# Performance work log

Measured on AMD Instinct MI355X. Metric: run time of the kernel, lower is better.

The kernel has to match this reference:

```python
import jax, jax.numpy as jnp
import numpy as np

H, W, C = 56, 56, 192
WS, SS = 7, 3          # window_size, shift_size
NH, HD = 6, 32         # num_heads, head_dim
N = WS * WS            # tokens per window = 49
HIDDEN = 4 * C
EPS = 1e-5


def _rel_pos_index():
    coords = np.stack(np.meshgrid(np.arange(WS), np.arange(WS), indexing='ij'))  # (2,ws,ws)
    flat = coords.reshape(2, -1)
    rel = flat[:, :, None] - flat[:, None, :]            # (2,N,N)
    rel = rel.transpose(1, 2, 0)
    rel[:, :, 0] += WS - 1
    rel[:, :, 1] += WS - 1
    rel[:, :, 0] *= 2 * WS - 1
    return rel.sum(-1)                                   # (N,N) int


def _attn_mask():
    img = np.zeros((H, W))
    cnt = 0
    for hs in (slice(0, -WS), slice(-WS, -SS), slice(-SS, None)):
        for ws_ in (slice(0, -WS), slice(-WS, -SS), slice(-SS, None)):
            img[hs, ws_] = cnt
            cnt += 1
    mw = img.reshape(H // WS, WS, W // WS, WS).transpose(0, 2, 1, 3).reshape(-1, N)  # (nW,N)
    diff = mw[:, None, :] - mw[:, :, None]
    return np.where(diff != 0, -100.0, 0.0).astype(np.float32)  # (nW,N,N)


REL_IDX = jnp.asarray(_rel_pos_index())
ATTN_MASK = jnp.asarray(_attn_mask())


def _ln(x, w, b):
    mu = x.mean(-1, keepdims=True)
    var = ((x - mu) ** 2).mean(-1, keepdims=True)
    return (x - mu) * jax.lax.rsqrt(var + EPS) * w + b


def _window_partition(x):
    # (B,H,W,C) -> (B*nW, N, C)
    B = x.shape[0]
    x = x.reshape(B, H // WS, WS, W // WS, WS, C)
    x = x.transpose(0, 1, 3, 2, 4, 5)
    return x.reshape(-1, N, C)


def _window_reverse(win, B):
    # (B*nW, N, C) -> (B,H,W,C)
    x = win.reshape(B, H // WS, W // WS, WS, WS, C)
    x = x.transpose(0, 1, 3, 2, 4, 5)
    return x.reshape(B, H, W, C)


def setup_inputs() -> dict:
    key = jax.random.key(0)
    ks = jax.random.split(key, 16)
    s = 0.02
    return {
        'x': jax.random.normal(ks[0], (64, H * W, C), jnp.float32),
        'norm1_w': jnp.ones((C,), jnp.float32),
        'norm1_b': jnp.zeros((C,), jnp.float32),
        'qkv_w': jax.random.normal(ks[1], (C, 3 * C), jnp.float32) * s,
        'qkv_b': jnp.zeros((3 * C,), jnp.float32),
        'rpb': jax.random.normal(ks[2], ((2 * WS - 1) ** 2, NH), jnp.float32) * s,
        'proj_w': jax.random.normal(ks[3], (C, C), jnp.float32) * s,
        'proj_b': jnp.zeros((C,), jnp.float32),
        'norm2_w': jnp.ones((C,), jnp.float32),
        'norm2_b': jnp.zeros((C,), jnp.float32),
        'fc1_w': jax.random.normal(ks[4], (C, HIDDEN), jnp.float32) * s,
        'fc1_b': jnp.zeros((HIDDEN,), jnp.float32),
        'fc2_w': jax.random.normal(ks[5], (HIDDEN, C), jnp.float32) * s,
        'fc2_b': jnp.zeros((C,), jnp.float32),
    }


def reference(x, norm1_w, norm1_b, qkv_w, qkv_b, rpb, proj_w, proj_b,
              norm2_w, norm2_b, fc1_w, fc1_b, fc2_w, fc2_b):
    B = x.shape[0]
    nW = (H // WS) * (W // WS)
    shortcut = x
    h = _ln(x, norm1_w, norm1_b).reshape(B, H, W, C)
    # cyclic shift
    h = jnp.roll(h, shift=(-SS, -SS), axis=(1, 2))
    xw = _window_partition(h)                                   # (B*nW, N, C)
    # windowed MHA
    qkv = (xw @ qkv_w + qkv_b).reshape(-1, N, 3, NH, HD).transpose(2, 0, 3, 1, 4)
    q, k, v = qkv[0], qkv[1], qkv[2]                            # (Bn, NH, N, HD)
    scale = HD ** -0.5
    attn = jnp.einsum('bhnd,bhmd->bhnm', q * scale, k)          # (Bn, NH, N, N)
    bias = rpb[REL_IDX.reshape(-1)].reshape(N, N, NH).transpose(2, 0, 1)
    attn = attn + bias[None]
    attn = attn.reshape(B, nW, NH, N, N) + ATTN_MASK[None, :, None]
    attn = jax.nn.softmax(attn.reshape(-1, NH, N, N), axis=-1)
    out = jnp.einsum('bhnm,bhmd->bhnd', attn, v)
    out = out.transpose(0, 2, 1, 3).reshape(-1, N, C)
    out = out @ proj_w + proj_b
    # reverse windows + un-shift
    h = _window_reverse(out, B)
    h = jnp.roll(h, shift=(SS, SS), axis=(1, 2)).reshape(B, H * W, C)
    x = shortcut + h
    # MLP (exact GELU, as torch nn.GELU default)
    m = _ln(x, norm2_w, norm2_b)
    m = jax.nn.gelu(m @ fc1_w + fc1_b, approximate=False)
    m = m @ fc2_w + fc2_b
    return x + m
```

## Files before the change

### kernel.cpp

```cpp
#include <hip/hip_runtime.h>
#include <hip/hip_bf16.h>

typedef __hip_bfloat16 bf16;
typedef __attribute__((ext_vector_type(8))) short short8;
typedef __attribute__((ext_vector_type(4))) float floatx4;

__device__ __forceinline__ floatx4 mfma16(short8 a, short8 b, floatx4 c) {
  return __builtin_amdgcn_mfma_f32_16x16x32_bf16(a, b, c, 0, 0, 0);
}

__device__ __forceinline__ float wave_sum(float v) {
#pragma unroll
  for (int off = 1; off < 64; off <<= 1) v += __shfl_xor(v, off);
  return v;
}

__global__ __launch_bounds__(256) void k_wt(const float* __restrict__ w,
                                            bf16* __restrict__ wt, int K, int N) {
  int id = blockIdx.x * 256 + threadIdx.x;
  if (id < K * N) {
    int n = id / K;
    int k = id - n * K;
    wt[id] = __float2bfloat16(w[(long)k * N + n]);
  }
}

template <bool GATHER>
__global__ __launch_bounds__(256) void k_ln(const float* __restrict__ xin,
                                            const float* __restrict__ w,
                                            const float* __restrict__ b,
                                            bf16* __restrict__ out) {
  const int lane = threadIdx.x & 63;
  const long row = (long)blockIdx.x * 4 + (threadIdx.x >> 6);
  long srow;
  if (GATHER) {
    int win = (int)(row / 49);
    int token = (int)(row - (long)win * 49);
    int bimg = win >> 6, wi = (win & 63) >> 3, wj = win & 7;
    int ti = token / 7, tj = token - ti * 7;
    int h = wi * 7 + ti + 3; if (h >= 56) h -= 56;
    int ww = wj * 7 + tj + 3; if (ww >= 56) ww -= 56;
    srow = (long)bimg * 3136 + h * 56 + ww;
  } else {
    srow = row;
  }
  const float* src = xin + srow * 192;
  float v0 = src[lane], v1 = src[lane + 64], v2 = src[lane + 128];
  float mu = wave_sum(v0 + v1 + v2) * (1.f / 192.f);
  float d0 = v0 - mu, d1 = v1 - mu, d2 = v2 - mu;
  float var = wave_sum(d0 * d0 + d1 * d1 + d2 * d2) * (1.f / 192.f);
  float rs = rsqrtf(var + 1e-5f);
  bf16* dst = out + row * 192;
  dst[lane]       = __float2bfloat16(d0 * rs * w[lane] + b[lane]);
  dst[lane + 64]  = __float2bfloat16(d1 * rs * w[lane + 64] + b[lane + 64]);
  dst[lane + 128] = __float2bfloat16(d2 * rs * w[lane + 128] + b[lane + 128]);
}

template <int EPI>
__global__ __launch_bounds__(256) void k_gemm(const bf16* __restrict__ A,
                                              const bf16* __restrict__ Bt,
                                              const float* __restrict__ bias,
                                              bf16* __restrict__ Cbf,
                                              float* __restrict__ Cfp,
                                              const float* __restrict__ res,
                                              int Ncols, int K, long row0) {
  __shared__ __align__(16) bf16 As[64 * 40];
  __shared__ __align__(16) bf16 Bs[64 * 40];
  const int t = threadIdx.x;
  const int lane = t & 63, wid = t >> 6;
  const int lanelo = lane & 15, quad = lane >> 4;
  const long m0 = (long)blockIdx.x * 64;
  const int n0 = blockIdx.y * 64;
  const int wm = (wid >> 1) * 32, wn = (wid & 1) * 32;
  const int srow = t >> 2, sch = (t & 3) * 8;

  floatx4 acc[2][2];
#pragma unroll
  for (int i = 0; i < 2; i++)
#pragma unroll
    for (int j = 0; j < 2; j++) acc[i][j] = (floatx4){0.f, 0.f, 0.f, 0.f};

  const bf16* Ap = A + (m0 + srow) * K + sch;
  const bf16* Bp = Bt + (long)(n0 + srow) * K + sch;

  for (int k0 = 0; k0 < K; k0 += 32) {
    __syncthreads();
    *(uint4*)(&As[srow * 40 + sch]) = *(const uint4*)(Ap + k0);
    *(uint4*)(&Bs[srow * 40 + sch]) = *(const uint4*)(Bp + k0);
    __syncthreads();
    short8 a0 = *(const short8*)(&As[(wm + lanelo) * 40 + quad * 8]);
    short8 a1 = *(const short8*)(&As[(wm + 16 + lanelo) * 40 + quad * 8]);
    short8 b0 = *(const short8*)(&Bs[(wn + lanelo) * 40 + quad * 8]);
    short8 b1 = *(const short8*)(&Bs[(wn + 16 + lanelo) * 40 + quad * 8]);
    acc[0][0] = mfma16(a0, b0, acc[0][0]);
    acc[0][1] = mfma16(a0, b1, acc[0][1]);
    acc[1][0] = mfma16(a1, b0, acc[1][0]);
    acc[1][1] = mfma16(a1, b1, acc[1][1]);
  }

#pragma unroll
  for (int mi = 0; mi < 2; mi++) {
#pragma unroll
    for (int reg = 0; reg < 4; reg++) {
      const long r = m0 + wm + mi * 16 + quad * 4 + reg;
      long orow = r;
      if (EPI == 2) {
        const long rg = row0 + r;
        int win = (int)(rg / 49);
        int token = (int)(rg - (long)win * 49);
        int bimg = win >> 6, wi = (win & 63) >> 3, wj = win & 7;
        int ti = token / 7, tj = token - ti * 7;
        int h = wi * 7 + ti + 3; if (h >= 56) h -= 56;
        int ww = wj * 7 + tj + 3; if (ww >= 56) ww -= 56;
        orow = (long)bimg * 3136 + h * 56 + ww;
      }
#pragma unroll
      for (int ni = 0; ni < 2; ni++) {
        const int c = n0 + wn + ni * 16 + lanelo;
        float v = acc[mi][ni][reg] + bias[c];
        if (EPI == 0) {
          Cbf[r * Ncols + c] = __float2bfloat16(v);
        } else if (EPI == 1) {
          v = 0.5f * v * (1.f + erff(v * 0.70710678118654752f));
          Cbf[r * Ncols + c] = __float2bfloat16(v);
        } else if (EPI == 2) {
          Cfp[orow * 192 + c] = v + res[orow * 192 + c];
        } else {
          Cfp[r * 192 + c] = v + res[r * 192 + c];
        }
      }
    }
  }
}

__global__ __launch_bounds__(256, 2) void k_attn(const bf16* __restrict__ qkv,
                                                 const float* __restrict__ rpb,
                                                 bf16* __restrict__ out) {
  __shared__ __align__(16) bf16 smem[4 * 7424];
  const int t = threadIdx.x, lane = t & 63, wid = t >> 6;
  const int lanelo = lane & 15, quad = lane >> 4;
  const int unit = blockIdx.x * 4 + wid;
  const int win = unit / 6, head = unit - win * 6;
  bf16* Qs = smem + wid * 7424;
  bf16* Ks = Qs + 2560;
  bf16* Vt = Qs + 5120;
  bf16* Ps = Qs;
  const long rowbase = (long)win * 49;
  const bf16* base = qkv + rowbase * 576 + head * 32;

  for (int idx = lane; idx < 196; idx += 64) {
    int tok = idx >> 2, ch = (idx & 3) * 8;
    *(uint4*)(&Qs[tok * 40 + ch]) = *(const uint4*)(base + (long)tok * 576 + ch);
    *(uint4*)(&Ks[tok * 40 + ch]) = *(const uint4*)(base + (long)tok * 576 + 192 + ch);
    union { uint4 u; bf16 h[8]; } tv;
    tv.u = *(const uint4*)(base + (long)tok * 576 + 384 + ch);
#pragma unroll
    for (int jj = 0; jj < 8; jj++) Vt[(ch + jj) * 72 + tok] = tv.h[jj];
  }
  for (int idx = lane; idx < 480; idx += 64) {
    int d = idx / 15, c = 49 + (idx - d * 15);
    Vt[d * 72 + c] = __float2bfloat16(0.f);
  }
  __syncthreads();

  floatx4 aS[4][4];
#pragma unroll
  for (int mi = 0; mi < 4; mi++)
#pragma unroll
    for (int ni = 0; ni < 4; ni++) aS[mi][ni] = (floatx4){0.f, 0.f, 0.f, 0.f};
  {
    short8 aq[4], bk[4];
#pragma unroll
    for (int mi = 0; mi < 4; mi++)
      aq[mi] = *(const short8*)(&Qs[(mi * 16 + lanelo) * 40 + quad * 8]);
#pragma unroll
    for (int ni = 0; ni < 4; ni++)
      bk[ni] = *(const short8*)(&Ks[(ni * 16 + lanelo) * 40 + quad * 8]);
#pragma unroll
    for (int mi = 0; mi < 4; mi++)
#pragma unroll
      for (int ni = 0; ni < 4; ni++) aS[mi][ni] = mfma16(aq[mi], bk[ni], aS[mi][ni]);
  }

  const int w_in = win & 63, wiw = w_in >> 3, wjw = w_in & 7;
  int cTi[4], cTj[4], cLab[4];
  bool cval[4];
#pragma unroll
  for (int ni = 0; ni < 4; ni++) {
    int j = ni * 16 + lanelo;
    cval[ni] = (j < 49);
    if (j > 48) j = 48;
    int ti = j / 7, tj = j - ti * 7;
    int rr = wiw * 7 + ti, cc = wjw * 7 + tj;
    cTi[ni] = ti;
    cTj[ni] = tj;
    cLab[ni] = ((rr < 49) ? 0 : (rr < 53 ? 1 : 2)) * 3 +
               ((cc < 49) ? 0 : (cc < 53 ? 1 : 2));
  }

  const float scale = 0.17677669529663687f;
  float rinv[16];
#pragma unroll
  for (int mi = 0; mi < 4; mi++) {
#pragma unroll
    for (int reg = 0; reg < 4; reg++) {
      int i = mi * 16 + quad * 4 + reg;
      if (i > 48) i = 48;
      int ti = i / 7, tj = i - ti * 7;
      int rr = wiw * 7 + ti, cc = wjw * 7 + tj;
      int rlab = ((rr < 49) ? 0 : (rr < 53 ? 1 : 2)) * 3 +
                 ((cc < 49) ? 0 : (cc < 53 ? 1 : 2));
      float sv[4];
      float mx = -1e30f;
#pragma unroll
      for (int ni = 0; ni < 4; ni++) {
        float s;
        if (cval[ni]) {
          int ridx = (ti - cTi[ni] + 6) * 13 + (tj - cTj[ni] + 6);
          float bb = rpb[ridx * 6 + head];
          if (rlab != cLab[ni]) bb -= 100.f;
          s = aS[mi][ni][reg] * scale + bb;
        } else {
          s = -1e30f;
        }
        sv[ni] = s;
        mx = fmaxf(mx, s);
      }
      mx = fmaxf(mx, __shfl_xor(mx, 1));
      mx = fmaxf(mx, __shfl_xor(mx, 2));
      mx = fmaxf(mx, __shfl_xor(mx, 4));
      mx = fmaxf(mx, __shfl_xor(mx, 8));
      float sum = 0.f;
#pragma unroll
      for (int ni = 0; ni < 4; ni++) {
        float p = __expf(sv[ni] - mx);
        sv[ni] = p;
        sum += p;
      }
      sum += __shfl_xor(sum, 1);
      sum += __shfl_xor(sum, 2);
      sum += __shfl_xor(sum, 4);
      sum += __shfl_xor(sum, 8);
      rinv[mi * 4 + reg] = 1.f / sum;
#pragma unroll
      for (int ni = 0; ni < 4; ni++) aS[mi][ni][reg] = sv[ni];
    }
  }
  __syncthreads();

#pragma unroll
  for (int mi = 0; mi < 4; mi++)
#pragma unroll
    for (int ni = 0; ni < 4; ni++)
#pragma unroll
      for (int reg = 0; reg < 4; reg++) {
        int i = mi * 16 + quad * 4 + reg, j = ni * 16 + lanelo;
        Ps[i * 72 + j] = __float2bfloat16(aS[mi][ni][reg]);
      }
  __syncthreads();

  floatx4 aO[4][2];
#pragma unroll
  for (int mi = 0; mi < 4; mi++)
#pragma unroll
    for (int ni = 0; ni < 2; ni++) aO[mi][ni] = (floatx4){0.f, 0.f, 0.f, 0.f};
#pragma unroll
  for (int k0 = 0; k0 < 64; k0 += 32) {
    short8 ap[4], bv[2];
#pragma unroll
    for (int mi = 0; mi < 4; mi++)
      ap[mi] = *(const short8*)(&Ps[(mi * 16 + lanelo) * 72 + k0 + quad * 8]);
#pragma unroll
    for (int ni = 0; ni < 2; ni++)
      bv[ni] = *(const short8*)(&Vt[(ni * 16 + lanelo) * 72 + k0 + quad * 8]);
#pragma unroll
    for (int mi = 0; mi < 4; mi++)
#pragma unroll
      for (int ni = 0; ni < 2; ni++) aO[mi][ni] = mfma16(ap[mi], bv[ni], aO[mi][ni]);
  }

#pragma unroll
  for (int mi = 0; mi < 4; mi++)
#pragma unroll
    for (int reg = 0; reg < 4; reg++) {
      int i = mi * 16 + quad * 4 + reg;
      if (i < 49) {
        float rv = rinv[mi * 4 + reg];
#pragma unroll
        for (int ni = 0; ni < 2; ni++) {
          int d = ni * 16 + lanelo;
          out[(rowbase + i) * 192 + head * 32 + d] =
              __float2bfloat16(aO[mi][ni][reg] * rv);
        }
      }
    }
}

extern "C" void kernel_launch(void* const* d_in, const int* in_sizes, int n_in,
                              void* d_out, int out_size, void* d_ws, size_t ws_size,
                              hipStream_t stream) {
  const float* x     = (const float*)d_in[0];
  const float* n1w   = (const float*)d_in[1];
  const float* n1b   = (const float*)d_in[2];
  const float* qkvw  = (const float*)d_in[3];
  const float* qkvb  = (const float*)d_in[4];
  const float* rpb   = (const float*)d_in[5];
  const float* projw = (const float*)d_in[6];
  const float* projb = (const float*)d_in[7];
  const float* n2w   = (const float*)d_in[8];
  const float* n2b   = (const float*)d_in[9];
  const float* fc1w  = (const float*)d_in[10];
  const float* fc1b  = (const float*)d_in[11];
  const float* fc2w  = (const float*)d_in[12];
  const float* fc2b  = (const float*)d_in[13];
  float* outf = (float*)d_out;

  const long CR = 50176;
  const int  NCH = 4;

  char* ws = (char*)d_ws;
  bf16* xw      = (bf16*)(ws + 0);
  bf16* qkvC    = (bf16*)(ws + 77070336LL);
  bf16* attC    = (bf16*)(ws + 134873088LL);
  bf16* hidC    = (bf16*)(ws + 77070336LL);
  bf16* m       = xw;
  bf16* wt_qkv  = (bf16*)(ws + 154140672LL);
  bf16* wt_proj = (bf16*)(ws + 154140672LL + 221184LL);
  bf16* wt_fc1  = (bf16*)(ws + 154140672LL + 294912LL);
  bf16* wt_fc2  = (bf16*)(ws + 154140672LL + 589824LL);

  k_wt<<<dim3((192 * 576 + 255) / 256), 256, 0, stream>>>(qkvw, wt_qkv, 192, 576);
  k_wt<<<dim3((192 * 192 + 255) / 256), 256, 0, stream>>>(projw, wt_proj, 192, 192);
  k_wt<<<dim3((192 * 768 + 255) / 256), 256, 0, stream>>>(fc1w, wt_fc1, 192, 768);
  k_wt<<<dim3((768 * 192 + 255) / 256), 256, 0, stream>>>(fc2w, wt_fc2, 768, 192);

  k_ln<true><<<dim3(50176), 256, 0, stream>>>(x, n1w, n1b, xw);

  for (int c = 0; c < NCH; c++) {
    const long r0 = c * CR;
    k_gemm<0><<<dim3(784, 9), 256, 0, stream>>>(xw + r0 * 192, wt_qkv, qkvb,
                                                qkvC, nullptr, nullptr, 576, 192, 0);
    k_attn<<<dim3(1536), 256, 0, stream>>>(qkvC, rpb, attC);
    k_gemm<2><<<dim3(784, 3), 256, 0, stream>>>(attC, wt_proj, projb, nullptr,
                                                outf, x, 192, 192, r0);
  }

  k_ln<false><<<dim3(50176), 256, 0, stream>>>(outf, n2w, n2b, m);

  for (int c = 0; c < NCH; c++) {
    const long r0 = c * CR;
    k_gemm<1><<<dim3(784, 12), 256, 0, stream>>>(m + r0 * 192, wt_fc1, fc1b,
                                                 hidC, nullptr, nullptr, 768, 192, 0);
    k_gemm<3><<<dim3(784, 3), 256, 0, stream>>>(hidC, wt_fc2, fc2b, nullptr,
                                                outf + r0 * 192, outf + r0 * 192,
                                                192, 768, 0);
  }
}
```

Measured before the change: 1.117 ms.

## Use direct global-to-LDS loads with wide K tiles and XOR-swizzled LDS in GEMM

The GEMM main loop now stages 64x192 bf16 tiles of A and B into LDS per iteration using the global_load_lds builtin, where it previously moved 64x32 tiles through registers. The LDS layout is XOR-swizzled to avoid bank conflicts, and the inner loop runs six MFMA k-steps per barrier pair. This cuts the number of synchronisations and the register-staging overhead. In exchange LDS use grows to 48KB per block with a 3-blocks-per-CU launch bound, and K must be a multiple of 192.

```diff
diff --git a/kernel.cpp b/kernel.cpp
--- a/kernel.cpp
+++ b/kernel.cpp
@@ -13,6 +13,16 @@
 #pragma unroll
   for (int off = 1; off < 64; off <<= 1) v += __shfl_xor(v, off);
   return v;
+}
+
+__device__ __forceinline__ void gload16(const void* g, void* l) {
+  __builtin_amdgcn_global_load_lds(
+      (const __attribute__((address_space(1))) unsigned int*)g,
+      (__attribute__((address_space(3))) unsigned int*)l, 16, 0, 0);
+}
+
+__device__ __forceinline__ short8 lds_frag(const char* base, int row, int kb) {
+  return *(const short8*)(base + row * 384 + (kb ^ ((row & 7) << 4)));
 }
 
 __global__ __launch_bounds__(256) void k_wt(const float* __restrict__ w,
@@ -57,22 +67,21 @@
 }
 
 template <int EPI>
-__global__ __launch_bounds__(256) void k_gemm(const bf16* __restrict__ A,
-                                              const bf16* __restrict__ Bt,
-                                              const float* __restrict__ bias,
-                                              bf16* __restrict__ Cbf,
-                                              float* __restrict__ Cfp,
-                                              const float* __restrict__ res,
-                                              int Ncols, int K, long row0) {
-  __shared__ __align__(16) bf16 As[64 * 40];
-  __shared__ __align__(16) bf16 Bs[64 * 40];
+__global__ __launch_bounds__(256, 3) void k_gemm(const bf16* __restrict__ A,
+                                                 const bf16* __restrict__ Bt,
+                                                 const float* __restrict__ bias,
+                                                 bf16* __restrict__ Cbf,
+                                                 float* __restrict__ Cfp,
+                                                 const float* __restrict__ res,
+                                                 int Ncols, int K, long row0) {
+  __shared__ __align__(16) char As[64 * 384];
+  __shared__ __align__(16) char Bs[64 * 384];
   const int t = threadIdx.x;
   const int lane = t & 63, wid = t >> 6;
   const int lanelo = lane & 15, quad = lane >> 4;
   const long m0 = (long)blockIdx.x * 64;
   const int n0 = blockIdx.y * 64;
   const int wm = (wid >> 1) * 32, wn = (wid & 1) * 32;
-  const int srow = t >> 2, sch = (t & 3) * 8;
 
   floatx4 acc[2][2];
 #pragma unroll
@@ -80,22 +89,35 @@
 #pragma unroll
     for (int j = 0; j < 2; j++) acc[i][j] = (floatx4){0.f, 0.f, 0.f, 0.f};
 
-  const bf16* Ap = A + (m0 + srow) * K + sch;
-  const bf16* Bp = Bt + (long)(n0 + srow) * K + sch;
-
-  for (int k0 = 0; k0 < K; k0 += 32) {
+  const char* Ab = (const char*)(A + m0 * (long)K);
+  const char* Bb = (const char*)(Bt + (long)n0 * K);
+  const int ldab = 2 * K;
+
+  for (int k0b = 0; k0b < 2 * K; k0b += 384) {
     __syncthreads();
-    *(uint4*)(&As[srow * 40 + sch]) = *(const uint4*)(Ap + k0);
-    *(uint4*)(&Bs[srow * 40 + sch]) = *(const uint4*)(Bp + k0);
+#pragma unroll
+    for (int i = 0; i < 6; i++) {
+      int c = i * 256 + t;
+      int r = c / 24;
+      int j = c - r * 24;
+      int be = (j * 16) ^ ((r & 7) << 4);
+      gload16(Ab + (long)r * ldab + k0b + be, As + c * 16);
+      gload16(Bb + (long)r * ldab + k0b + be, Bs + c * 16);
+    }
     __syncthreads();
-    short8 a0 = *(const short8*)(&As[(wm + lanelo) * 40 + quad * 8]);
-    short8 a1 = *(const short8*)(&As[(wm + 16 + lanelo) * 40 + quad * 8]);
-    short8 b0 = *(const short8*)(&Bs[(wn + lanelo) * 40 + quad * 8]);
-    short8 b1 = *(const short8*)(&Bs[(wn + 16 + lanelo) * 40 + quad * 8]);
-    acc[0][0] = mfma16(a0, b0, acc[0][0]);
-    acc[0][1] = mfma16(a0, b1, acc[0][1]);
-    acc[1][0] = mfma16(a1, b0, acc[1][0]);
-    acc[1][1] = mfma16(a1, b1, acc[1][1]);
+
+#pragma unroll
+    for (int kk = 0; kk < 6; kk++) {
+      const int kb = kk * 64 + quad * 16;
+      short8 a0 = lds_frag(As, wm + lanelo, kb);
+      short8 a1 = lds_frag(As, wm + 16 + lanelo, kb);
+      short8 b0 = lds_frag(Bs, wn + lanelo, kb);
+      short8 b1 = lds_frag(Bs, wn + 16 + lanelo, kb);
+      acc[0][0] = mfma16(a0, b0, acc[0][0]);
+      acc[0][1] = mfma16(a0, b1, acc[0][1]);
+      acc[1][0] = mfma16(a1, b0, acc[1][0]);
+      acc[1][1] = mfma16(a1, b1, acc[1][1]);
+    }
   }
 
 #pragma unroll
```

Measured after the change: 1.097 ms. No clear change (-1.8%).
